# Performance work log

Measured on AMD Instinct MI355X. Metric: run time of the kernel, lower is better.

## Reference

```python
import jax, jax.numpy as jnp
import numpy as np


def _rel_pos_table(size, rel_pos):
    # q_size == k_size, fixed_input_size=True -> no interpolation, lambda=1
    coords = jnp.arange(size)[:, None] - jnp.arange(size)[None, :] + (size - 1)
    return rel_pos[coords]  # (size, size, head_dim)


def setup_inputs() -> dict:
    key = jax.random.key(0)
    ks = jax.random.split(key, 7)
    N, H, W, C = 8, 32, 32, 768
    hd = C // 12
    return {
        "x": jax.random.normal(ks[0], (N, H, W, C), jnp.float32),
        "w_qkv": jax.random.normal(ks[1], (C, 3 * C), jnp.float32) * 0.02,
        "b_qkv": jax.random.normal(ks[2], (3 * C,), jnp.float32) * 0.02,
        "w_proj": jax.random.normal(ks[3], (C, C), jnp.float32) * 0.02,
        "b_proj": jax.random.normal(ks[4], (C,), jnp.float32) * 0.02,
        "rel_pos_h": jax.random.normal(ks[5], (2 * H - 1, hd), jnp.float32) * 0.02,
        "rel_pos_w": jax.random.normal(ks[6], (2 * W - 1, hd), jnp.float32) * 0.02,
        "nb_heads": 12,
    }


def reference(x, w_qkv, b_qkv, w_proj, b_proj, rel_pos_h, rel_pos_w, nb_heads):
    N, H, W, C = x.shape
    hd = C // nb_heads
    scale = hd ** -0.5
    HW = H * W

    qkv = x.reshape(N, HW, C) @ w_qkv + b_qkv            # (N, HW, 3C)
    qkv = qkv.reshape(N, HW, 3, nb_heads, hd)
    qkv = jnp.transpose(qkv, (2, 0, 3, 1, 4)).reshape(3, N * nb_heads, HW, hd)
    q, k, v = qkv[0], qkv[1], qkv[2]

    attn = jnp.einsum('bqd,bkd->bqk', q, k) * scale      # (N*heads, HW, HW)

    # decomposed relative position bias (MViTv2)
    r_h = _rel_pos_table(H, rel_pos_h)                   # (H, H, hd)
    r_w = _rel_pos_table(W, rel_pos_w)                   # (W, W, hd)
    q4 = q.reshape(N * nb_heads, H, W, hd)
    bias_h = jnp.einsum('nhwc,hkc->nhwk', q4, r_h)       # (B, H, W, H)
    bias_w = jnp.einsum('nhwc,wkc->nhwk', q4, r_w)       # (B, H, W, W)
    attn = attn.reshape(N * nb_heads, H, W, H, W)
    attn = attn + bias_h[..., :, None] + bias_w[..., None, :]
    attn = attn.reshape(N * nb_heads, HW, HW)

    attn = jax.nn.softmax(attn, axis=-1)
    out = jnp.einsum('bqk,bkd->bqd', attn, v)            # (N*heads, HW, hd)
    out = out.reshape(N, nb_heads, H, W, hd)
    out = jnp.transpose(out, (0, 2, 3, 1, 4)).reshape(N, H, W, C)
    return out @ w_proj + b_proj
```

## Files before the change

kernel.cpp:

```cpp
#include <hip/hip_runtime.h>
#include <hip/hip_bf16.h>

#define N_    8
#define H_    32
#define W_    32
#define C_    768
#define NH_   12
#define HD_   64
#define B_    96
#define HW_   1024
#define C3_   2304
#define SCALE_ 0.125f
#define LOG2E_ 1.4426950408889634f

typedef __attribute__((ext_vector_type(4))) float f32x4;
typedef __attribute__((ext_vector_type(16))) float f32x16;
typedef __attribute__((ext_vector_type(8))) short s16x8;
typedef __attribute__((ext_vector_type(2))) int i32x2;
typedef __attribute__((ext_vector_type(2))) unsigned int u32x2;
typedef __attribute__((ext_vector_type(4))) unsigned int u32x4;
typedef unsigned short u16;
typedef unsigned int u32;

__device__ inline u16 f2b(float x) {
    __hip_bfloat16 h = __float2bfloat16(x);
    return *reinterpret_cast<u16*>(&h);
}
__device__ inline float b2f(u16 x) {
    u32 u = ((u32)x) << 16;
    return *reinterpret_cast<float*>(&u);
}

__device__ __forceinline__ void gld_lds16(const void* g, void* l) {
    __builtin_amdgcn_global_load_lds(
        (const __attribute__((address_space(1))) u32*)g,
        (__attribute__((address_space(3))) u32*)l, 16, 0, 0);
}

__global__ __launch_bounds__(256) void cvt_bf16(const float* __restrict__ in,
                                                u16* __restrict__ out, int n4) {
    for (int i = blockIdx.x * blockDim.x + threadIdx.x; i < n4; i += gridDim.x * blockDim.x) {
        float4 v = ((const float4*)in)[i];
        ushort4 o;
        o.x = f2b(v.x); o.y = f2b(v.y); o.z = f2b(v.z); o.w = f2b(v.w);
        ((ushort4*)out)[i] = o;
    }
}

__global__ __launch_bounds__(256) void tcvt_bf16(const float* __restrict__ in,
                                                 u16* __restrict__ out, int K, int N) {
    __shared__ u16 tile[64][72];
    const int t = threadIdx.x;
    const int k0 = blockIdx.y * 64, n0 = blockIdx.x * 64;
    const int r = t >> 2, c4 = (t & 3) * 16;
    #pragma unroll
    for (int u = 0; u < 4; ++u) {
        float4 v = *(const float4*)(in + (size_t)(k0 + r) * N + n0 + c4 + u * 4);
        tile[c4 + u*4 + 0][r] = f2b(v.x);
        tile[c4 + u*4 + 1][r] = f2b(v.y);
        tile[c4 + u*4 + 2][r] = f2b(v.z);
        tile[c4 + u*4 + 3][r] = f2b(v.w);
    }
    __syncthreads();
    #pragma unroll
    for (int u = 0; u < 2; ++u) {
        s16x8 v;
        #pragma unroll
        for (int e = 0; e < 8; ++e) v[e] = (short)tile[r][c4 + u*8 + e];
        *(s16x8*)(out + (size_t)(n0 + r) * K + k0 + c4 + u*8) = v;
    }
}

__global__ __launch_bounds__(256) void gemm_qkv(const u16* __restrict__ A,
                                                const u16* __restrict__ Bt,
                                                const float* __restrict__ bias,
                                                u16* __restrict__ qout,
                                                u16* __restrict__ kout,
                                                u16* __restrict__ vout) {
    extern __shared__ char smem[];
    u16* sA = (u16*)smem;
    u16* sB = (u16*)(smem + 16384);
    u16* T  = (u16*)smem;

    const int t = threadIdx.x;
    const int lane = t & 63;
    const int w = t >> 6;
    const int wm = w >> 1, wn = w & 1;
    const int l15 = lane & 15, lg = lane >> 4;
    const int nbase = blockIdx.x * 128;
    const int mbase = blockIdx.y * 128;
    const int srow = lane >> 2;
    const int sslot = lane & 3;
    const u16* gA0 = A + (size_t)(mbase + w * 16 + srow) * 768 + sslot * 8;
    const u16* gA1 = gA0 + (size_t)64 * 768;
    const u16* gB0 = Bt + (size_t)(nbase + w * 16 + srow) * 768 + sslot * 8;
    const u16* gB1 = gB0 + (size_t)64 * 768;
    f32x4 acc[4][4] = {};
    gld_lds16(gA0, sA + w * 512);
    gld_lds16(gA1, sA + (w + 4) * 512);
    gld_lds16(gB0, sB + w * 512);
    gld_lds16(gB1, sB + (w + 4) * 512);
    for (int kt = 0; kt < 24; ++kt) {
        const int p = kt & 1;
        __syncthreads();
        if (kt < 23) {
            const int kb = (kt + 1) * 32;
            gld_lds16(gA0 + kb, sA + (p ^ 1) * 4096 + w * 512);
            gld_lds16(gA1 + kb, sA + (p ^ 1) * 4096 + (w + 4) * 512);
            gld_lds16(gB0 + kb, sB + (p ^ 1) * 4096 + w * 512);
            gld_lds16(gB1 + kb, sB + (p ^ 1) * 4096 + (w + 4) * 512);
        }
        const u16* pa = sA + p * 4096 + (wm * 64 + l15) * 32 + lg * 8;
        const u16* pb = sB + p * 4096 + (wn * 64 + l15) * 32 + lg * 8;
        s16x8 afr[4], bfr[4];
        #pragma unroll
        for (int i = 0; i < 4; ++i) {
            afr[i] = *(const s16x8*)(pa + i * 512);
            bfr[i] = *(const s16x8*)(pb + i * 512);
        }
        #pragma unroll
        for (int i = 0; i < 4; ++i)
            #pragma unroll
            for (int j = 0; j < 4; ++j)
                acc[i][j] = __builtin_amdgcn_mfma_f32_16x16x32_bf16(afr[i], bfr[j],
                                                                    acc[i][j], 0, 0, 0);
    }

    const int which = nbase / C_;
    const int head0 = (nbase % C_) >> 6;
    const int n_img = mbase >> 10;
    const int pbase = mbase & 1023;
    __syncthreads();

    if (which < 2) {
        #pragma unroll
        for (int i = 0; i < 4; ++i)
            #pragma unroll
            for (int r = 0; r < 4; ++r) {
                const int lm = wm * 64 + i * 16 + lg * 4 + r;
                #pragma unroll
                for (int j = 0; j < 4; ++j) {
                    const int lc = wn * 64 + j * 16 + l15;
                    T[lm * 136 + lc] = f2b(acc[i][j][r] + bias[nbase + lc]);
                }
            }
    } else {
        #pragma unroll
        for (int i = 0; i < 4; ++i)
            #pragma unroll
            for (int r = 0; r < 4; ++r) {
                const int lm = wm * 64 + i * 16 + lg * 4 + r;
                #pragma unroll
                for (int j = 0; j < 4; ++j) {
                    const int lc = wn * 64 + j * 16 + l15;
                    T[lc * 136 + lm] = f2b(acc[i][j][r] + bias[nbase + lc]);
                }
            }
    }
    __syncthreads();

    if (which < 2) {
        u16* dst = (which == 0) ? qout : kout;
        #pragma unroll
        for (int pass = 0; pass < 4; ++pass) {
            const int lm = pass * 32 + (t >> 3);
            #pragma unroll
            for (int hh = 0; hh < 2; ++hh) {
                s16x8 row = *(const s16x8*)(T + lm * 136 + hh * 64 + (t & 7) * 8);
                const size_t bidx = (size_t)(n_img * NH_ + head0 + hh);
                *(s16x8*)(dst + (bidx * HW_ + pbase + lm) * HD_ + (t & 7) * 8) = row;
            }
        }
    } else {
        #pragma unroll
        for (int pass = 0; pass < 8; ++pass) {
            const int lc = pass * 16 + (t >> 4);
            s16x8 row = *(const s16x8*)(T + lc * 136 + (t & 15) * 8);
            const int hh = lc >> 6, d = lc & 63;
            const size_t bidx = (size_t)(n_img * NH_ + head0 + hh);
            *(s16x8*)(vout + bidx * (size_t)(HW_ * HD_) + (size_t)d * HW_ + pbase + (t & 15) * 8) = row;
        }
    }
}

#define GEMM_CORE(A_, Bt_)                                                           \
    __shared__ u16 sA[2][128 * 32];                                                  \
    __shared__ u16 sB[2][128 * 32];                                                  \
    const int t = threadIdx.x;                                                       \
    const int lane = t & 63;                                                         \
    const int w = t >> 6;                                                            \
    const int wm = w >> 1, wn = w & 1;                                               \
    const int l15 = lane & 15, lg = lane >> 4;                                       \
    const int nbase = blockIdx.x * 128;                                              \
    const int mbase = blockIdx.y * 128;                                              \
    const int srow = lane >> 2;                                                      \
    const int sslot = lane & 3;                                                      \
    const u16* gA0 = (A_) + (size_t)(mbase + w * 16 + srow) * 768 + sslot * 8;       \
    const u16* gA1 = gA0 + (size_t)64 * 768;                                         \
    const u16* gB0 = (Bt_) + (size_t)(nbase + w * 16 + srow) * 768 + sslot * 8;      \
    const u16* gB1 = gB0 + (size_t)64 * 768;                                         \
    f32x4 acc[4][4] = {};                                                            \
    gld_lds16(gA0, &sA[0][w * 512]);                                                 \
    gld_lds16(gA1, &sA[0][(w + 4) * 512]);                                           \
    gld_lds16(gB0, &sB[0][w * 512]);                                                 \
    gld_lds16(gB1, &sB[0][(w + 4) * 512]);                                           \
    for (int kt = 0; kt < 24; ++kt) {                                                \
        const int p = kt & 1;                                                        \
        __syncthreads();                                                             \
        if (kt < 23) {                                                               \
            const int kb = (kt + 1) * 32;                                            \
            gld_lds16(gA0 + kb, &sA[p ^ 1][w * 512]);                                \
            gld_lds16(gA1 + kb, &sA[p ^ 1][(w + 4) * 512]);                          \
            gld_lds16(gB0 + kb, &sB[p ^ 1][w * 512]);                                \
            gld_lds16(gB1 + kb, &sB[p ^ 1][(w + 4) * 512]);                          \
        }                                                                            \
        const u16* pa = &sA[p][(wm * 64 + l15) * 32 + lg * 8];                       \
        const u16* pb = &sB[p][(wn * 64 + l15) * 32 + lg * 8];                       \
        s16x8 afr[4], bfr[4];                                                        \
        _Pragma("unroll")                                                            \
        for (int i = 0; i < 4; ++i) {                                                \
            afr[i] = *(const s16x8*)(pa + i * 512);                                  \
            bfr[i] = *(const s16x8*)(pb + i * 512);                                  \
        }                                                                            \
        _Pragma("unroll")                                                            \
        for (int i = 0; i < 4; ++i)                                                  \
            _Pragma("unroll")                                                        \
            for (int j = 0; j < 4; ++j)                                              \
                acc[i][j] = __builtin_amdgcn_mfma_f32_16x16x32_bf16(afr[i], bfr[j],  \
                                                                    acc[i][j], 0, 0, 0); \
    }

__global__ __launch_bounds__(256) void gemm_proj(const u16* __restrict__ A,
                                                 const u16* __restrict__ Bt,
                                                 const float* __restrict__ bias,
                                                 float* __restrict__ out) {
    GEMM_CORE(A, Bt)
    const int mrow0 = mbase + wm * 64 + lg * 4;
    #pragma unroll
    for (int i = 0; i < 4; ++i) {
        #pragma unroll
        for (int r = 0; r < 4; ++r) {
            const int m = mrow0 + i * 16 + r;
            #pragma unroll
            for (int j = 0; j < 4; ++j) {
                const int n = nbase + wn * 64 + j * 16 + l15;
                out[(size_t)m * C_ + n] = acc[i][j][r] + bias[n];
            }
        }
    }
}

__global__ __launch_bounds__(256) void ef_gemm(const u16* __restrict__ qb_,
                                               const float* __restrict__ rel_h,
                                               const float* __restrict__ rel_w,
                                               u16* __restrict__ Fg,
                                               u16* __restrict__ Eg) {
    const int t = threadIdx.x;
    const int lane = t & 63;
    const int w = t >> 6;
    const int l31 = lane & 31;
    const int hi  = lane >> 5;
    const size_t Mrow = (size_t)blockIdx.x * 128 + w * 32 + l31;

    s16x8 qb[4];
    {
        const u16* qrow = qb_ + Mrow * HD_;
        #pragma unroll
        for (int ck = 0; ck < 4; ++ck)
            qb[ck] = *(const s16x8*)(qrow + ck * 16 + hi * 8);
    }

    #pragma unroll
    for (int tb = 0; tb < 2; ++tb) {
        const float* R = tb ? rel_w : rel_h;
        u16* og = (tb ? Eg : Fg) + Mrow * 64;
        #pragma unroll
        for (int hh = 0; hh < 2; ++hh) {
            const int dr = hh * 32 + l31;
            const float* rrow = R + (size_t)(dr > 62 ? 62 : dr) * HD_;
            f32x16 acc = {};
            #pragma unroll
            for (int ck = 0; ck < 4; ++ck) {
                float4 r0 = *(const float4*)(rrow + ck * 16 + hi * 8);
                float4 r1 = *(const float4*)(rrow + ck * 16 + hi * 8 + 4);
                s16x8 af;
                af[0] = (short)f2b(r0.x * LOG2E_); af[1] = (short)f2b(r0.y * LOG2E_);
                af[2] = (short)f2b(r0.z * LOG2E_); af[3] = (short)f2b(r0.w * LOG2E_);
                af[4] = (short)f2b(r1.x * LOG2E_); af[5] = (short)f2b(r1.y * LOG2E_);
                af[6] = (short)f2b(r1.z * LOG2E_); af[7] = (short)f2b(r1.w * LOG2E_);
                acc = __builtin_amdgcn_mfma_f32_32x32x16_bf16(af, qb[ck], acc, 0, 0, 0);
            }
            #pragma unroll
            for (int u = 0; u < 4; ++u) {
                u32x2 pkd;
                pkd.x = (u32)f2b(acc[4*u+0]) | ((u32)f2b(acc[4*u+1]) << 16);
                pkd.y = (u32)f2b(acc[4*u+2]) | ((u32)f2b(acc[4*u+3]) << 16);
                *(u32x2*)(og + hh * 32 + u * 8 + 4 * hi) = pkd;
            }
        }
    }
}

__global__ __launch_bounds__(256) void attn_mfma(const u16* __restrict__ qb_,
                                                 const u16* __restrict__ kbf,
                                                 const u16* __restrict__ vtb,
                                                 const u16* __restrict__ Fg,
                                                 const u16* __restrict__ Eg,
                                                 u16* __restrict__ ob) {
    extern __shared__ char smem[];
    u16*   sBH  = (u16*)smem;
    u16*   sK0  = (u16*)(smem + 8704);
    u16*   sK1  = (u16*)(smem + 17920);
    u16*   sVt0 = (u16*)(smem + 27136);
    u16*   sVt1 = (u16*)(smem + 36352);

    const int t = threadIdx.x;
    const int lane = t & 63;
    const int w = t >> 6;
    const int l31 = lane & 31;
    const int hi  = lane >> 5;
    const int qw  = w * 32;

    const int bid = blockIdx.x;
    const int swz = (bid & 7) * 96 + (bid >> 3);
    const int b = swz >> 3;
    const int qbase = (swz & 7) * 128;

    s16x8 qfr[4];
    {
        const u16* qrow = qb_ + ((size_t)b * HW_ + qbase + qw + l31) * HD_;
        #pragma unroll
        for (int ck = 0; ck < 4; ++ck) {
            s16x8 qv = *(const s16x8*)(qrow + ck * 16 + hi * 8);
            #pragma unroll
            for (int e = 0; e < 8; ++e)
                qfr[ck][e] = (short)f2b(b2f((u16)qv[e]) * (SCALE_ * LOG2E_));
        }
    }

    {
        const u16* Fb = Fg + (size_t)b * HW_ * 64;
        for (int idv = t; idv < 4096; idv += 256) {
            const int row = idv >> 5;
            const int kh  = idv & 31;
            const int qg  = qbase + row;
            sBH[row * 34 + kh] = Fb[(size_t)qg * 64 + (qg >> 5) + 31 - kh];
        }
    }

    f32x4 bwv[4];
    {
        const int qmy = qbase + qw + l31;
        const u16* Erow = Eg + (size_t)(b * HW_ + qmy) * 64;
        #pragma unroll
        for (int m = 0; m < 4; ++m)
            #pragma unroll
            for (int j = 0; j < 4; ++j)
                bwv[m][j] = b2f(Erow[l31 + 31 - (m * 8 + 4 * hi + j)]);
    }

    const int srow = t >> 2;
    const int sc0  = (t & 3) * 16;
    const u16* kg = kbf + ((size_t)b * HW_ + srow) * HD_ + sc0;
    const u16* vg = vtb + (size_t)b * HD_ * HW_ + (size_t)srow * HW_ + sc0;
    u16* skw0 = sK0  + srow * 72 + sc0;
    u16* skw1 = sK1  + srow * 72 + sc0;
    u16* svw0 = sVt0 + srow * 72 + sc0;
    u16* svw1 = sVt1 + srow * 72 + sc0;

    s16x8 kr0 = *(const s16x8*)(kg);
    s16x8 kr1 = *(const s16x8*)(kg + 8);
    s16x8 vr0 = *(const s16x8*)(vg);
    s16x8 vr1 = *(const s16x8*)(vg + 8);
    *(s16x8*)(skw0)     = kr0;
    *(s16x8*)(skw0 + 8) = kr1;
    *(s16x8*)(svw0)     = vr0;
    *(s16x8*)(svw0 + 8) = vr1;
    __syncthreads();

    f32x16 Oacc[2] = {};
    float lsum = 0.f;
    const int bhbase = (qw + l31) * 34;

    auto body = [&](int kt, const u16* sKr, const u16* sVr, u16* skwN, u16* svwN) {
        if (kt < 15) {
            const u16* kn = kg + (size_t)(kt + 1) * 64 * HD_;
            kr0 = *(const s16x8*)(kn);
            kr1 = *(const s16x8*)(kn + 8);
            const u16* vn = vg + (size_t)(kt + 1) * 64;
            vr0 = *(const s16x8*)(vn);
            vr1 = *(const s16x8*)(vn + 8);
        }

        const float bh0 = b2f(sBH[bhbase + 2 * kt]);
        const float bh1 = b2f(sBH[bhbase + 2 * kt + 1]);

        #pragma unroll
        for (int kvt = 0; kvt < 2; ++kvt) {
            f32x16 s = {};
            __builtin_amdgcn_s_setprio(1);
            #pragma unroll
            for (int ck = 0; ck < 4; ++ck) {
                s16x8 kf = *(const s16x8*)(sKr + (kvt * 32 + l31) * 72 + ck * 16 + hi * 8);
                s = __builtin_amdgcn_mfma_f32_32x32x16_bf16(kf, qfr[ck], s, 0, 0, 0);
            }
            __builtin_amdgcn_s_setprio(0);
            const float bh = kvt ? bh1 : bh0;

            u32 pw[8];
            #pragma unroll
            for (int m = 0; m < 8; ++m) {
                float p0 = __builtin_amdgcn_exp2f(s[2*m]   + bh + bwv[(2*m)>>2][(2*m)&3]);
                float p1 = __builtin_amdgcn_exp2f(s[2*m+1] + bh + bwv[(2*m+1)>>2][(2*m+1)&3]);
                lsum += p0 + p1;
                pw[m] = (u32)f2b(p0) | ((u32)f2b(p1) << 16);
            }

            __builtin_amdgcn_s_setprio(1);
            #pragma unroll
            for (int cc = 0; cc < 2; ++cc) {
                i32x2 s02 = __builtin_amdgcn_permlane32_swap((int)pw[cc*4+0], (int)pw[cc*4+2], false, false);
                i32x2 s13 = __builtin_amdgcn_permlane32_swap((int)pw[cc*4+1], (int)pw[cc*4+3], false, false);
                u32x4 pau;
                pau.x = (u32)s02.x; pau.y = (u32)s13.x;
                pau.z = (u32)s02.y; pau.w = (u32)s13.y;
                s16x8 pa = *reinterpret_cast<s16x8*>(&pau);
                const int kc = kvt * 2 + cc;
                #pragma unroll
                for (int dt = 0; dt < 2; ++dt) {
                    s16x8 vf = *(const s16x8*)(sVr + (dt * 32 + l31) * 72 + kc * 16 + hi * 8);
                    Oacc[dt] = __builtin_amdgcn_mfma_f32_32x32x16_bf16(pa, vf, Oacc[dt], 0, 0, 0);
                }
            }
            __builtin_amdgcn_s_setprio(0);
        }

        if (kt < 15) {
            *(s16x8*)(skwN)     = kr0;
            *(s16x8*)(skwN + 8) = kr1;
            *(s16x8*)(svwN)     = vr0;
            *(s16x8*)(svwN + 8) = vr1;
        }
        asm volatile("s_waitcnt lgkmcnt(0)" ::: "memory");
        __builtin_amdgcn_s_barrier();
        __builtin_amdgcn_sched_barrier(0);
    };

    for (int k2 = 0; k2 < 8; ++k2) {
        body(2 * k2,     sK0, sVt0, skw1, svw1);
        body(2 * k2 + 1, sK1, sVt1, skw0, svw0);
    }

    float lsumF = lsum + __shfl_xor(lsum, 32);
    float linv[16];
    #pragma unroll
    for (int r = 0; r < 16; ++r) {
        const int qloc = (r & 3) + 8 * (r >> 2) + 4 * hi;
        linv[r] = 1.0f / __shfl(lsumF, qloc);
    }

    const int n_img = b / NH_;
    const int head  = b % NH_;
    #pragma unroll
    for (int dt = 0; dt < 2; ++dt) {
        #pragma unroll
        for (int r = 0; r < 16; ++r) {
            const int qloc = (r & 3) + 8 * (r >> 2) + 4 * hi;
            const int qg = qbase + qw + qloc;
            ob[(size_t)(n_img * HW_ + qg) * C_ + head * HD_ + dt * 32 + l31] =
                f2b(Oacc[dt][r] * linv[r]);
        }
    }
}

extern "C" void kernel_launch(void* const* d_in, const int* in_sizes, int n_in,
                              void* d_out, int out_size, void* d_ws, size_t ws_size,
                              hipStream_t stream) {
    const float* x      = (const float*)d_in[0];
    const float* w_qkv  = (const float*)d_in[1];
    const float* b_qkv  = (const float*)d_in[2];
    const float* w_proj = (const float*)d_in[3];
    const float* b_proj = (const float*)d_in[4];
    const float* rel_h  = (const float*)d_in[5];
    const float* rel_w  = (const float*)d_in[6];
    float* out = (float*)d_out;

    const size_t seg = (size_t)B_ * HW_ * HD_;
    char* p = (char*)d_ws;
    u16* xb     = (u16*)p;  p += seg * 2;
    u16* wqkvT  = (u16*)p;  p += (size_t)C3_ * C_ * 2;
    u16* wprojT = (u16*)p;  p += (size_t)C_ * C_ * 2;
    u16* qb     = (u16*)p;  p += seg * 2;
    u16* kbf    = (u16*)p;  p += seg * 2;
    u16* vtb    = (u16*)p;  p += seg * 2;
    u16* ob     = (u16*)p;  p += seg * 2;
    u16* Fg     = (u16*)p;  p += seg * 2;
    u16* Eg     = (u16*)p;  p += seg * 2;

    cvt_bf16<<<2048, 256, 0, stream>>>(x, xb, (int)(seg / 4));
    tcvt_bf16<<<dim3(C3_ / 64, C_ / 64), 256, 0, stream>>>(w_qkv, wqkvT, C_, C3_);
    tcvt_bf16<<<dim3(C_ / 64, C_ / 64), 256, 0, stream>>>(w_proj, wprojT, C_, C_);

    gemm_qkv<<<dim3(C3_ / 128, 8192 / 128), 256, 34816, stream>>>(xb, wqkvT, b_qkv, qb, kbf, vtb);
    ef_gemm<<<768, 256, 0, stream>>>(qb, rel_h, rel_w, Fg, Eg);
    attn_mfma<<<768, 256, 45568, stream>>>(qb, kbf, vtb, Fg, Eg, ob);
    gemm_proj<<<dim3(C_ / 128, 8192 / 128), 256, 0, stream>>>(ob, wprojT, b_proj, out);
}
```

Measured before the change: 160.4 us.

## Triple-buffer GEMM LDS pipeline with vmcnt waits and XCD-aware block swizzle

Both projection GEMMs now share a 3-stage LDS ring in place of double buffering. Explicit s_waitcnt vmcnt(4) plus raw s_barrier let two K-tiles stay in flight while one is computed, hiding more global-load latency. The grid becomes 1D with a swizzle that groups consecutive tiles per XCD (blockIdx&7) to improve L2 reuse. This costs more LDS per block (48KB), which may reduce occupancy, and the hand-written waitcnt/barrier sequencing is fragile.

```diff
diff --git a/kernel.cpp b/kernel.cpp
--- a/kernel.cpp
+++ b/kernel.cpp
@@ -71,151 +71,16 @@
     }
 }
 
-__global__ __launch_bounds__(256) void gemm_qkv(const u16* __restrict__ A,
-                                                const u16* __restrict__ Bt,
-                                                const float* __restrict__ bias,
-                                                u16* __restrict__ qout,
-                                                u16* __restrict__ kout,
-                                                u16* __restrict__ vout) {
-    extern __shared__ char smem[];
-    u16* sA = (u16*)smem;
-    u16* sB = (u16*)(smem + 16384);
-    u16* T  = (u16*)smem;
-
-    const int t = threadIdx.x;
-    const int lane = t & 63;
-    const int w = t >> 6;
-    const int wm = w >> 1, wn = w & 1;
-    const int l15 = lane & 15, lg = lane >> 4;
-    const int nbase = blockIdx.x * 128;
-    const int mbase = blockIdx.y * 128;
-    const int srow = lane >> 2;
-    const int sslot = lane & 3;
-    const u16* gA0 = A + (size_t)(mbase + w * 16 + srow) * 768 + sslot * 8;
-    const u16* gA1 = gA0 + (size_t)64 * 768;
-    const u16* gB0 = Bt + (size_t)(nbase + w * 16 + srow) * 768 + sslot * 8;
-    const u16* gB1 = gB0 + (size_t)64 * 768;
-    f32x4 acc[4][4] = {};
-    gld_lds16(gA0, sA + w * 512);
-    gld_lds16(gA1, sA + (w + 4) * 512);
-    gld_lds16(gB0, sB + w * 512);
-    gld_lds16(gB1, sB + (w + 4) * 512);
-    for (int kt = 0; kt < 24; ++kt) {
-        const int p = kt & 1;
-        __syncthreads();
-        if (kt < 23) {
-            const int kb = (kt + 1) * 32;
-            gld_lds16(gA0 + kb, sA + (p ^ 1) * 4096 + w * 512);
-            gld_lds16(gA1 + kb, sA + (p ^ 1) * 4096 + (w + 4) * 512);
-            gld_lds16(gB0 + kb, sB + (p ^ 1) * 4096 + w * 512);
-            gld_lds16(gB1 + kb, sB + (p ^ 1) * 4096 + (w + 4) * 512);
-        }
-        const u16* pa = sA + p * 4096 + (wm * 64 + l15) * 32 + lg * 8;
-        const u16* pb = sB + p * 4096 + (wn * 64 + l15) * 32 + lg * 8;
-        s16x8 afr[4], bfr[4];
-        #pragma unroll
-        for (int i = 0; i < 4; ++i) {
-            afr[i] = *(const s16x8*)(pa + i * 512);
-            bfr[i] = *(const s16x8*)(pb + i * 512);
-        }
-        #pragma unroll
-        for (int i = 0; i < 4; ++i)
-            #pragma unroll
-            for (int j = 0; j < 4; ++j)
-                acc[i][j] = __builtin_amdgcn_mfma_f32_16x16x32_bf16(afr[i], bfr[j],
-                                                                    acc[i][j], 0, 0, 0);
-    }
-
-    const int which = nbase / C_;
-    const int head0 = (nbase % C_) >> 6;
-    const int n_img = mbase >> 10;
-    const int pbase = mbase & 1023;
-    __syncthreads();
-
-    if (which < 2) {
-        #pragma unroll
-        for (int i = 0; i < 4; ++i)
-            #pragma unroll
-            for (int r = 0; r < 4; ++r) {
-                const int lm = wm * 64 + i * 16 + lg * 4 + r;
-                #pragma unroll
-                for (int j = 0; j < 4; ++j) {
-                    const int lc = wn * 64 + j * 16 + l15;
-                    T[lm * 136 + lc] = f2b(acc[i][j][r] + bias[nbase + lc]);
-                }
-            }
-    } else {
-        #pragma unroll
-        for (int i = 0; i < 4; ++i)
-            #pragma unroll
-            for (int r = 0; r < 4; ++r) {
-                const int lm = wm * 64 + i * 16 + lg * 4 + r;
-                #pragma unroll
-                for (int j = 0; j < 4; ++j) {
-                    const int lc = wn * 64 + j * 16 + l15;
-                    T[lc * 136 + lm] = f2b(acc[i][j][r] + bias[nbase + lc]);
-                }
-            }
-    }
-    __syncthreads();
-
-    if (which < 2) {
-        u16* dst = (which == 0) ? qout : kout;
-        #pragma unroll
-        for (int pass = 0; pass < 4; ++pass) {
-            const int lm = pass * 32 + (t >> 3);
-            #pragma unroll
-            for (int hh = 0; hh < 2; ++hh) {
-                s16x8 row = *(const s16x8*)(T + lm * 136 + hh * 64 + (t & 7) * 8);
-                const size_t bidx = (size_t)(n_img * NH_ + head0 + hh);
-                *(s16x8*)(dst + (bidx * HW_ + pbase + lm) * HD_ + (t & 7) * 8) = row;
-            }
-        }
-    } else {
-        #pragma unroll
-        for (int pass = 0; pass < 8; ++pass) {
-            const int lc = pass * 16 + (t >> 4);
-            s16x8 row = *(const s16x8*)(T + lc * 136 + (t & 15) * 8);
-            const int hh = lc >> 6, d = lc & 63;
-            const size_t bidx = (size_t)(n_img * NH_ + head0 + hh);
-            *(s16x8*)(vout + bidx * (size_t)(HW_ * HD_) + (size_t)d * HW_ + pbase + (t & 15) * 8) = row;
-        }
-    }
-}
-
-#define GEMM_CORE(A_, Bt_)                                                           \
-    __shared__ u16 sA[2][128 * 32];                                                  \
-    __shared__ u16 sB[2][128 * 32];                                                  \
-    const int t = threadIdx.x;                                                       \
-    const int lane = t & 63;                                                         \
-    const int w = t >> 6;                                                            \
-    const int wm = w >> 1, wn = w & 1;                                               \
-    const int l15 = lane & 15, lg = lane >> 4;                                       \
-    const int nbase = blockIdx.x * 128;                                              \
-    const int mbase = blockIdx.y * 128;                                              \
-    const int srow = lane >> 2;                                                      \
-    const int sslot = lane & 3;                                                      \
-    const u16* gA0 = (A_) + (size_t)(mbase + w * 16 + srow) * 768 + sslot * 8;       \
-    const u16* gA1 = gA0 + (size_t)64 * 768;                                         \
-    const u16* gB0 = (Bt_) + (size_t)(nbase + w * 16 + srow) * 768 + sslot * 8;      \
-    const u16* gB1 = gB0 + (size_t)64 * 768;                                         \
-    f32x4 acc[4][4] = {};                                                            \
-    gld_lds16(gA0, &sA[0][w * 512]);                                                 \
-    gld_lds16(gA1, &sA[0][(w + 4) * 512]);                                           \
-    gld_lds16(gB0, &sB[0][w * 512]);                                                 \
-    gld_lds16(gB1, &sB[0][(w + 4) * 512]);                                           \
-    for (int kt = 0; kt < 24; ++kt) {                                                \
-        const int p = kt & 1;                                                        \
-        __syncthreads();                                                             \
-        if (kt < 23) {                                                               \
-            const int kb = (kt + 1) * 32;                                            \
-            gld_lds16(gA0 + kb, &sA[p ^ 1][w * 512]);                                \
-            gld_lds16(gA1 + kb, &sA[p ^ 1][(w + 4) * 512]);                          \
-            gld_lds16(gB0 + kb, &sB[p ^ 1][w * 512]);                                \
-            gld_lds16(gB1 + kb, &sB[p ^ 1][(w + 4) * 512]);                          \
-        }                                                                            \
-        const u16* pa = &sA[p][(wm * 64 + l15) * 32 + lg * 8];                       \
-        const u16* pb = &sB[p][(wn * 64 + l15) * 32 + lg * 8];                       \
+#define G3_ISSUE(KB, BUF)                                                            \
+    gld_lds16(gA0 + (KB), sAb + (BUF) * 4096 + w * 512);                             \
+    gld_lds16(gA1 + (KB), sAb + (BUF) * 4096 + (w + 4) * 512);                       \
+    gld_lds16(gB0 + (KB), sBb + (BUF) * 4096 + w * 512);                             \
+    gld_lds16(gB1 + (KB), sBb + (BUF) * 4096 + (w + 4) * 512);
+
+#define G3_COMP(BUF)                                                                 \
+    {                                                                                \
+        const u16* pa = sAb + (BUF) * 4096 + (wm * 64 + l15) * 32 + lg * 8;          \
+        const u16* pb = sBb + (BUF) * 4096 + (wn * 64 + l15) * 32 + lg * 8;          \
         s16x8 afr[4], bfr[4];                                                        \
         _Pragma("unroll")                                                            \
         for (int i = 0; i < 4; ++i) {                                                \
@@ -230,11 +95,119 @@
                                                                     acc[i][j], 0, 0, 0); \
     }
 
+#define G3_BAR4                                                                      \
+    asm volatile("s_waitcnt vmcnt(4) lgkmcnt(0)" ::: "memory");                      \
+    __builtin_amdgcn_s_barrier();                                                    \
+    __builtin_amdgcn_sched_barrier(0);
+
+#define G3_BAR0                                                                      \
+    asm volatile("s_waitcnt vmcnt(0) lgkmcnt(0)" ::: "memory");                      \
+    __builtin_amdgcn_s_barrier();                                                    \
+    __builtin_amdgcn_sched_barrier(0);
+
+#define GEMM_CORE3(A_, Bt_, NT_)                                                     \
+    extern __shared__ char smem[];                                                   \
+    u16* sAb = (u16*)smem;                                     \
+    u16* sBb = (u16*)(smem + 24576);                           \
+    const int t = threadIdx.x;                                                       \
+    const int lane = t & 63;                                                         \
+    const int w = t >> 6;                                                            \
+    const int wm = w >> 1, wn = w & 1;                                               \
+    const int l15 = lane & 15, lg = lane >> 4;                                       \
+    const int per = (int)gridDim.x >> 3;                                             \
+    const int swz = ((int)blockIdx.x & 7) * per + ((int)blockIdx.x >> 3);            \
+    const int nbase = (swz % (NT_)) * 128;                                           \
+    const int mbase = (swz / (NT_)) * 128;                                           \
+    const int srow = lane >> 2;                                                      \
+    const int sslot = lane & 3;                                                      \
+    const u16* gA0 = (A_) + (size_t)(mbase + w * 16 + srow) * 768 + sslot * 8;       \
+    const u16* gA1 = gA0 + (size_t)64 * 768;                                         \
+    const u16* gB0 = (Bt_) + (size_t)(nbase + w * 16 + srow) * 768 + sslot * 8;      \
+    const u16* gB1 = gB0 + (size_t)64 * 768;                                         \
+    f32x4 acc[4][4] = {};                                                            \
+    G3_ISSUE(0, 0)                                                                   \
+    G3_ISSUE(32, 1)                                                                  \
+    G3_BAR4                                   \
+    for (int k3 = 0; k3 < 7; ++k3) {                                                 \
+        const int kb = k3 * 96;                                                      \
+        G3_ISSUE(kb + 64, 2)  G3_COMP(0)  G3_BAR4                                    \
+        G3_ISSUE(kb + 96, 0)  G3_COMP(1)  G3_BAR4                                    \
+        G3_ISSUE(kb + 128, 1) G3_COMP(2)  G3_BAR4                                    \
+    }                                                                                \
+    G3_ISSUE(736, 2) G3_COMP(0) G3_BAR4                        \
+    G3_COMP(1) G3_BAR0                                         \
+    G3_COMP(2) G3_BAR0
+
+__global__ __launch_bounds__(256) void gemm_qkv(const u16* __restrict__ A,
+                                                const u16* __restrict__ Bt,
+                                                const float* __restrict__ bias,
+                                                u16* __restrict__ qout,
+                                                u16* __restrict__ kout,
+                                                u16* __restrict__ vout) {
+    GEMM_CORE3(A, Bt, 18)
+    u16* T = (u16*)smem;
+
+    const int which = nbase / C_;
+    const int head0 = (nbase % C_) >> 6;
+    const int n_img = mbase >> 10;
+    const int pbase = mbase & 1023;
+
+    if (which < 2) {
+        #pragma unroll
+        for (int i = 0; i < 4; ++i)
+            #pragma unroll
+            for (int r = 0; r < 4; ++r) {
+                const int lm = wm * 64 + i * 16 + lg * 4 + r;
+                #pragma unroll
+                for (int j = 0; j < 4; ++j) {
+                    const int lc = wn * 64 + j * 16 + l15;
+                    T[lm * 136 + lc] = f2b(acc[i][j][r] + bias[nbase + lc]);
+                }
+            }
+    } else {
+        #pragma unroll
+        for (int i = 0; i < 4; ++i)
+            #pragma unroll
+            for (int r = 0; r < 4; ++r) {
+                const int lm = wm * 64 + i * 16 + lg * 4 + r;
+                #pragma unroll
+                for (int j = 0; j < 4; ++j) {
+                    const int lc = wn * 64 + j * 16 + l15;
+                    T[lc * 136 + lm] = f2b(acc[i][j][r] + bias[nbase + lc]);
+                }
+            }
+    }
+    __syncthreads();
+
+    if (which < 2) {
+        u16* dst = (which == 0) ? qout : kout;
+        #pragma unroll
+        for (int pass = 0; pass < 4; ++pass) {
+            const int lm = pass * 32 + (t >> 3);
+            #pragma unroll
+            for (int hh = 0; hh < 2; ++hh) {
+                s16x8 row = *(const s16x8*)(T + lm * 136 + hh * 64 + (t & 7) * 8);
+                const size_t bidx = (size_t)(n_img * NH_ + head0 + hh);
+                *(s16x8*)(dst + (bidx * HW_ + pbase + lm) * HD_ + (t & 7) * 8) = row;
+            }
+        }
+    } else {
+        #pragma unroll
+        for (int pass = 0; pass < 8; ++pass) {
+            const int lc = pass * 16 + (t >> 4);
+            s16x8 row = *(const s16x8*)(T + lc * 136 + (t & 15) * 8);
+            const int hh = lc >> 6, d = lc & 63;
+            const size_t bidx = (size_t)(n_img * NH_ + head0 + hh);
+            *(s16x8*)(vout + bidx * (size_t)(HW_ * HD_) + (size_t)d * HW_ + pbase + (t & 15) * 8) = row;
+        }
+    }
+}
+
 __global__ __launch_bounds__(256) void gemm_proj(const u16* __restrict__ A,
                                                  const u16* __restrict__ Bt,
                                                  const float* __restrict__ bias,
                                                  float* __restrict__ out) {
-    GEMM_CORE(A, Bt)
+    GEMM_CORE3(A, Bt, 6)
     const int mrow0 = mbase + wm * 64 + lg * 4;
     #pragma unroll
     for (int i = 0; i < 4; ++i) {
@@ -501,8 +474,8 @@
     tcvt_bf16<<<dim3(C3_ / 64, C_ / 64), 256, 0, stream>>>(w_qkv, wqkvT, C_, C3_);
     tcvt_bf16<<<dim3(C_ / 64, C_ / 64), 256, 0, stream>>>(w_proj, wprojT, C_, C_);
 
-    gemm_qkv<<<dim3(C3_ / 128, 8192 / 128), 256, 34816, stream>>>(xb, wqkvT, b_qkv, qb, kbf, vtb);
+    gemm_qkv<<<1152, 256, 49152, stream>>>(xb, wqkvT, b_qkv, qb, kbf, vtb);
     ef_gemm<<<768, 256, 0, stream>>>(qb, rel_h, rel_w, Fg, Eg);
     attn_mfma<<<768, 256, 45568, stream>>>(qb, kbf, vtb, Fg, Eg, ob);
-    gemm_proj<<<dim3(C_ / 128, 8192 / 128), 256, 0, stream>>>(ob, wprojT, b_proj, out);
-}
+    gemm_proj<<<384, 256, 49152, stream>>>(ob, wprojT, b_proj, out);
+}
```

After: 142.8 us. -11.0%, faster.
